# Optimization experiments

Hardware: AMD Instinct MI355X
Metric: run time of the kernel (lower is better)

Reference implementation:

```python
import jax, jax.numpy as jnp
import numpy as np

HID = 512
HEADS = 8
HD = HID // HEADS  # 64


def setup_inputs() -> dict:
    key = jax.random.key(0)
    ks = jax.random.split(key, 16)
    B, LQ, LK = 2, 384, 384
    s_in = 1.0 / np.sqrt(HID)
    s_hd = 1.0 / np.sqrt(HD)
    return {
        "query": jax.random.normal(ks[0], (B, LQ, HID), jnp.float32),
        "key":   jax.random.normal(ks[1], (B, LK, HID), jnp.float32),
        "value": jax.random.normal(ks[2], (B, LK, HID), jnp.float32),
        # linear weights stored as (in, out) so y = x @ W + b
        "Wq": jax.random.uniform(ks[3], (HID, HID), jnp.float32, -s_in, s_in),
        "bq": jnp.zeros((HID,), jnp.float32),
        "Wk": jax.random.uniform(ks[4], (HID, HID), jnp.float32, -s_in, s_in),
        "bk": jnp.zeros((HID,), jnp.float32),
        "Wv": jax.random.uniform(ks[5], (HID, HID), jnp.float32, -s_in, s_in),
        "bv": jnp.zeros((HID,), jnp.float32),
        "Ww": jax.random.uniform(ks[6], (HD, HD), jnp.float32, -s_hd, s_hd),
        "bw": jnp.zeros((HD,), jnp.float32),
        "Wu": jax.random.uniform(ks[7], (HD, HD), jnp.float32, -s_hd, s_hd),
        "bu": jnp.zeros((HD,), jnp.float32),
        "vv": jax.random.uniform(ks[8], (HD,), jnp.float32, -s_hd, s_hd),
        "Wo": jax.random.uniform(ks[9], (HID, HID), jnp.float32, -s_in, s_in),
        "bo": jnp.zeros((HID,), jnp.float32),
    }


def reference(query, key, value, Wq, bq, Wk, bk, Wv, bv, Ww, bw, Wu, bu, vv, Wo, bo):
    B, LQ, _ = query.shape
    LK = key.shape[1]
    scale = jnp.sqrt(jnp.asarray(HD, query.dtype))

    def split_heads(x, L):
        return x.reshape(B, L, HEADS, HD).transpose(0, 2, 1, 3)  # [B,H,L,hd]

    Q = split_heads(query @ Wq + bq, LQ)
    K = split_heads(key @ Wk + bk, LK)
    V = split_heads(value @ Wv + bv, LK)

    qW = Q @ Ww + bw            # [B,H,Lq,hd]
    kU = K @ Wu + bu            # [B,H,Lk,hd]
    # additive energy: tanh(W(Q)+U(K)) . vv  -> [B,H,Lq,Lk]
    e = jnp.tanh(qW[:, :, :, None, :] + kU[:, :, None, :, :])  # [B,H,Lq,Lk,hd]
    energy = jnp.einsum('bhqkd,d->bhqk', e, vv) / scale

    attention = jax.nn.softmax(energy, axis=-1)
    x = jnp.einsum('bhqk,bhkd->bhqd', attention, V)
    x = x.transpose(0, 2, 1, 3).reshape(B, LQ, HID)
    x = x @ Wo + bo
    return (x, attention)
```

## Files before the change

### kernel.cpp

```cpp
#include <hip/hip_runtime.h>

#define HID 512
#define HEADS 8
#define HD 64
#define BATCH 2
#define SEQ 384
#define MROWS (BATCH * SEQ)
#define KT_N 48
#define APACK_S8 (48 * KT_N * 64)
#define BPACK_S8 (32 * KT_N * 64)

#define C1 2.8853900817779268f
#define SSCL 0.18033688011112043f

typedef __attribute__((ext_vector_type(8))) short s8v;
typedef __attribute__((ext_vector_type(4))) float f4v;

__device__ __forceinline__ unsigned short bf16_rne(float x) {
    union { float f; unsigned u; } v; v.f = x;
    unsigned r = v.u + 0x7FFFu + ((v.u >> 16) & 1u);
    return (unsigned short)(r >> 16);
}
__device__ __forceinline__ float bf16_val(unsigned short h) {
    union { float f; unsigned u; } v; v.u = ((unsigned)h) << 16; return v.f;
}

__global__ __launch_bounds__(256) void prep_kernel(
    const float* __restrict__ Wq, const float* __restrict__ bq,
    const float* __restrict__ Wk, const float* __restrict__ bk,
    const float* __restrict__ Ww, const float* __restrict__ bw,
    const float* __restrict__ Wu, const float* __restrict__ bu,
    const float* __restrict__ vv,
    float* __restrict__ wqe, float* __restrict__ wke,
    float* __restrict__ bqe, float* __restrict__ bke,
    float* __restrict__ vv2)
{
    int tid = blockIdx.x * 256 + threadIdx.x;
    if (tid < 262144) {
        int i = tid >> 9, n = tid & 511, h = n >> 6, j = n & 63;
        const float* wrow = Wq + i * HID + h * HD;
        float s = 0.f;
        #pragma unroll 8
        for (int t = 0; t < 64; ++t) s = fmaf(wrow[t], Ww[t * 64 + j], s);
        wqe[tid] = s;
    } else if (tid < 524288) {
        int idx = tid - 262144;
        int i = idx >> 9, n = idx & 511, h = n >> 6, j = n & 63;
        const float* wrow = Wk + i * HID + h * HD;
        float s = 0.f;
        #pragma unroll 8
        for (int t = 0; t < 64; ++t) s = fmaf(wrow[t], Wu[t * 64 + j], s);
        wke[idx] = s;
    } else if (tid < 524800) {
        int n = tid - 524288, h = n >> 6, j = n & 63;
        float s = bw[j];
        for (int t = 0; t < 64; ++t) s = fmaf(bq[h * 64 + t], Ww[t * 64 + j], s);
        bqe[n] = s;
    } else if (tid < 525312) {
        int n = tid - 524800, h = n >> 6, j = n & 63;
        float s = bu[j];
        for (int t = 0; t < 64; ++t) s = fmaf(bk[h * 64 + t], Wu[t * 64 + j], s);
        bke[n] = s;
    } else if (tid < 525376) {
        int d = tid - 525312;
        vv2[d] = -2.0f * vv[d];
    }
}

__device__ __forceinline__ void pack_a_one(const float* __restrict__ src,
                                           s8v* __restrict__ dst, int rem)
{
    int g = rem & 63, m = rem >> 6;
    const float4* sp = (const float4*)(src + (size_t)m * HID + g * 8);
    float4 v0 = sp[0], v1 = sp[1];
    float vals[8] = {v0.x, v0.y, v0.z, v0.w, v1.x, v1.y, v1.z, v1.w};
    s8v hi, lo;
    #pragma unroll
    for (int j = 0; j < 8; ++j) {
        unsigned short h = bf16_rne(vals[j]);
        hi[j] = (short)h;
        lo[j] = (short)bf16_rne(vals[j] - bf16_val(h));
    }
    int mt = m >> 4, kt = g >> 2;
    int lanei = (m & 15) | ((g & 3) << 4);
    size_t base = ((size_t)mt * KT_N) * 64 + lanei;
    dst[base + (size_t)kt * 64]        = hi;
    dst[base + (size_t)(16 + kt) * 64] = hi;
    dst[base + (size_t)(32 + kt) * 64] = lo;
}

__global__ __launch_bounds__(256) void pack_a3_kernel(
    const float* __restrict__ q, const float* __restrict__ k, const float* __restrict__ v,
    s8v* __restrict__ Aq, s8v* __restrict__ Ak, s8v* __restrict__ Av)
{
    int bx = blockIdx.x;
    int p = bx / 192;
    int rem = (bx % 192) * 256 + threadIdx.x;
    const float* src = (p == 0) ? q : (p == 1) ? k : v;
    s8v* dst = (p == 0) ? Aq : (p == 1) ? Ak : Av;
    pack_a_one(src, dst, rem);
}

__global__ __launch_bounds__(256) void pack_a1_kernel(
    const float* __restrict__ x, s8v* __restrict__ Ax)
{
    pack_a_one(x, Ax, blockIdx.x * 256 + threadIdx.x);
}

__device__ __forceinline__ void pack_w_one(const float* __restrict__ W,
                                           s8v* __restrict__ dst, int rem)
{
    int kg = rem >> 9, n = rem & 511;
    s8v hi, lo;
    #pragma unroll
    for (int j = 0; j < 8; ++j) {
        float x = W[(size_t)(kg * 8 + j) * HID + n];
        unsigned short h = bf16_rne(x);
        hi[j] = (short)h;
        lo[j] = (short)bf16_rne(x - bf16_val(h));
    }
    int nt = n >> 4, kt = kg >> 2;
    int lanei = (n & 15) | ((kg & 3) << 4);
    size_t base = ((size_t)nt * KT_N) * 64 + lanei;
    dst[base + (size_t)kt * 64]        = hi;
    dst[base + (size_t)(16 + kt) * 64] = lo;
    dst[base + (size_t)(32 + kt) * 64] = hi;
}

__global__ __launch_bounds__(256) void pack_w_kernel(
    const float* __restrict__ w0, const float* __restrict__ w1,
    const float* __restrict__ w2, const float* __restrict__ w3,
    s8v* __restrict__ B0, s8v* __restrict__ B1,
    s8v* __restrict__ B2, s8v* __restrict__ B3)
{
    int bx = blockIdx.x;
    int p = bx >> 7;
    int rem = (bx & 127) * 256 + threadIdx.x;
    const float* W = (p == 0) ? w0 : (p == 1) ? w1 : (p == 2) ? w2 : w3;
    s8v* dst = (p == 0) ? B0 : (p == 1) ? B1 : (p == 2) ? B2 : B3;
    pack_w_one(W, dst, rem);
}

template <int MODE>
__device__ __forceinline__ void mfma_gemm_body(
    const s8v* __restrict__ Ap, const s8v* __restrict__ Bp,
    const float* __restrict__ bias, float* __restrict__ out,
    int bm, int bn)
{
    int tid = threadIdx.x;
    int w = __builtin_amdgcn_readfirstlane(tid >> 6);
    int lane = tid & 63;
    int mt0 = bm * 4 + (w & 1) * 2;
    int nt0 = bn * 4 + (w >> 1) * 2;

    const s8v* a0p = Ap + (size_t)(mt0 * KT_N) * 64 + lane;
    const s8v* a1p = a0p + (size_t)KT_N * 64;
    const s8v* b0p = Bp + (size_t)(nt0 * KT_N) * 64 + lane;
    const s8v* b1p = b0p + (size_t)KT_N * 64;

    f4v acc00 = {0.f, 0.f, 0.f, 0.f};
    f4v acc01 = {0.f, 0.f, 0.f, 0.f};
    f4v acc10 = {0.f, 0.f, 0.f, 0.f};
    f4v acc11 = {0.f, 0.f, 0.f, 0.f};

    s8v xa0 = a0p[0], xa1 = a1p[0], xb0 = b0p[0], xb1 = b1p[0];
    #pragma unroll 1
    for (int kt = 0; kt < KT_N; kt += 2) {
        int o1 = (kt + 1) * 64;
        s8v ya0 = a0p[o1], ya1 = a1p[o1], yb0 = b0p[o1], yb1 = b1p[o1];
        acc00 = __builtin_amdgcn_mfma_f32_16x16x32_bf16(xa0, xb0, acc00, 0, 0, 0);
        acc01 = __builtin_amdgcn_mfma_f32_16x16x32_bf16(xa0, xb1, acc01, 0, 0, 0);
        acc10 = __builtin_amdgcn_mfma_f32_16x16x32_bf16(xa1, xb0, acc10, 0, 0, 0);
        acc11 = __builtin_amdgcn_mfma_f32_16x16x32_bf16(xa1, xb1, acc11, 0, 0, 0);
        int o2 = (kt + 2 < KT_N) ? (kt + 2) * 64 : 0;
        xa0 = a0p[o2]; xa1 = a1p[o2]; xb0 = b0p[o2]; xb1 = b1p[o2];
        acc00 = __builtin_amdgcn_mfma_f32_16x16x32_bf16(ya0, yb0, acc00, 0, 0, 0);
        acc01 = __builtin_amdgcn_mfma_f32_16x16x32_bf16(ya0, yb1, acc01, 0, 0, 0);
        acc10 = __builtin_amdgcn_mfma_f32_16x16x32_bf16(ya1, yb0, acc10, 0, 0, 0);
        acc11 = __builtin_amdgcn_mfma_f32_16x16x32_bf16(ya1, yb1, acc11, 0, 0, 0);
    }

    int quad = lane >> 4, c16 = lane & 15;
    int col0 = nt0 * 16 + c16, col1 = col0 + 16;
    float bias0 = bias[col0], bias1 = bias[col1];
    int row0 = mt0 * 16 + quad * 4;
    int row1 = row0 + 16;

    #pragma unroll
    for (int r = 0; r < 4; ++r) {
        float y;
        #define WR(ROW, COL, Y)                                                     \
        {                                                                           \
            float yy = (Y);                                                         \
            if (MODE != 0) yy = __builtin_amdgcn_exp2f(C1 * yy);                    \
            if (MODE == 2) {                                                        \
                int b2 = (ROW) / SEQ, kk = (ROW) - b2 * SEQ;                        \
                int hh = (COL) >> 6, dd = (COL) & 63;                               \
                out[(((size_t)((b2 * 8 + hh) * 16 + (dd >> 2)) * SEQ + kk) << 2)    \
                    + (dd & 3)] = yy;                                               \
            } else {                                                                \
                out[(size_t)(ROW) * HID + (COL)] = yy;                              \
            }                                                                       \
        }
        y = acc00[r] + bias0; WR(row0 + r, col0, y);
        y = acc01[r] + bias1; WR(row0 + r, col1, y);
        y = acc10[r] + bias0; WR(row1 + r, col0, y);
        y = acc11[r] + bias1; WR(row1 + r, col1, y);
        #undef WR
    }
}

__global__ __launch_bounds__(256) void proj3_mfma_kernel(
    const s8v* __restrict__ Aq, const s8v* __restrict__ Ak, const s8v* __restrict__ Av,
    const s8v* __restrict__ Bq, const s8v* __restrict__ Bk, const s8v* __restrict__ Bv,
    const float* __restrict__ bqe, const float* __restrict__ bke, const float* __restrict__ bv,
    float* __restrict__ Eq, float* __restrict__ Ek4, float* __restrict__ V)
{
    int p = blockIdx.z;
    if (p == 0)      mfma_gemm_body<1>(Aq, Bq, bqe, Eq,  blockIdx.x, blockIdx.y);
    else if (p == 1) mfma_gemm_body<2>(Ak, Bk, bke, Ek4, blockIdx.x, blockIdx.y);
    else             mfma_gemm_body<0>(Av, Bv, bv,  V,   blockIdx.x, blockIdx.y);
}

__global__ __launch_bounds__(256) void out_mfma_kernel(
    const s8v* __restrict__ Ax, const s8v* __restrict__ Bo,
    const float* __restrict__ bo, float* __restrict__ out)
{
    mfma_gemm_body<0>(Ax, Bo, bo, out, blockIdx.x, blockIdx.y);
}

__global__ __launch_bounds__(256, 6) void attn_kernel(
    const float* __restrict__ Eq, const float* __restrict__ Ek4,
    const float* __restrict__ V, const float* __restrict__ vv2,
    float* __restrict__ attnOut, float* __restrict__ X)
{
    __shared__ float aP[4][SEQ];

    int bh = blockIdx.y;
    int b = bh >> 3, h = bh & 7;
    int tid = threadIdx.x;
    int wave = __builtin_amdgcn_readfirstlane(tid >> 6);
    int lane = tid & 63;
    int q = blockIdx.x * 4 + wave;

    const float* eqrow = Eq + (size_t)(b * SEQ + q) * HID + h * HD;
    const float4* ekbase = (const float4*)Ek4 + (size_t)bh * 16 * SEQ + lane;

    float e[6];
    #pragma unroll
    for (int kt = 0; kt < 6; ++kt) e[kt] = 0.f;

    #pragma unroll 1
    for (int c = 0; c < 4; ++c) {
        float g[16], w[16];
        #pragma unroll
        for (int j = 0; j < 16; ++j) {
            g[j] = eqrow[c * 16 + j];
            w[j] = vv2[c * 16 + j];
        }
        const float4* ekc = ekbase + (size_t)c * 4 * SEQ;
        #pragma unroll
        for (int kt = 0; kt < 6; ++kt) {
            const float4* ekp = ekc + kt * 64;
            float4 k0 = ekp[0 * SEQ];
            float4 k1 = ekp[1 * SEQ];
            float4 k2 = ekp[2 * SEQ];
            float4 k3 = ekp[3 * SEQ];
            float r = e[kt];
            r = fmaf(w[0],  __builtin_amdgcn_rcpf(fmaf(g[0],  k0.x, 1.f)), r);
            r = fmaf(w[1],  __builtin_amdgcn_rcpf(fmaf(g[1],  k0.y, 1.f)), r);
            r = fmaf(w[2],  __builtin_amdgcn_rcpf(fmaf(g[2],  k0.z, 1.f)), r);
            r = fmaf(w[3],  __builtin_amdgcn_rcpf(fmaf(g[3],  k0.w, 1.f)), r);
            r = fmaf(w[4],  __builtin_amdgcn_rcpf(fmaf(g[4],  k1.x, 1.f)), r);
            r = fmaf(w[5],  __builtin_amdgcn_rcpf(fmaf(g[5],  k1.y, 1.f)), r);
            r = fmaf(w[6],  __builtin_amdgcn_rcpf(fmaf(g[6],  k1.z, 1.f)), r);
            r = fmaf(w[7],  __builtin_amdgcn_rcpf(fmaf(g[7],  k1.w, 1.f)), r);
            r = fmaf(w[8],  __builtin_amdgcn_rcpf(fmaf(g[8],  k2.x, 1.f)), r);
            r = fmaf(w[9],  __builtin_amdgcn_rcpf(fmaf(g[9],  k2.y, 1.f)), r);
            r = fmaf(w[10], __builtin_amdgcn_rcpf(fmaf(g[10], k2.z, 1.f)), r);
            r = fmaf(w[11], __builtin_amdgcn_rcpf(fmaf(g[11], k2.w, 1.f)), r);
            r = fmaf(w[12], __builtin_amdgcn_rcpf(fmaf(g[12], k3.x, 1.f)), r);
            r = fmaf(w[13], __builtin_amdgcn_rcpf(fmaf(g[13], k3.y, 1.f)), r);
            r = fmaf(w[14], __builtin_amdgcn_rcpf(fmaf(g[14], k3.z, 1.f)), r);
            r = fmaf(w[15], __builtin_amdgcn_rcpf(fmaf(g[15], k3.w, 1.f)), r);
            e[kt] = r;
        }
    }

    float m = e[0];
    #pragma unroll
    for (int t = 1; t < 6; ++t) m = fmaxf(m, e[t]);
    #pragma unroll
    for (int off = 1; off < 64; off <<= 1) m = fmaxf(m, __shfl_xor(m, off));
    float a[6], s = 0.f;
    #pragma unroll
    for (int t = 0; t < 6; ++t) {
        a[t] = __builtin_amdgcn_exp2f((e[t] - m) * SSCL);
        s += a[t];
    }
    #pragma unroll
    for (int off = 1; off < 64; off <<= 1) s += __shfl_xor(s, off);
    float z = __builtin_amdgcn_rcpf(s);

    size_t abase = (size_t)bh * SEQ * SEQ + (size_t)q * SEQ;
    #pragma unroll
    for (int t = 0; t < 6; ++t) {
        float av = a[t] * z;
        attnOut[abase + t * 64 + lane] = av;
        aP[wave][t * 64 + lane] = av;
    }

    int ko = lane >> 4, d4p = lane & 15;
    const float4* vb = (const float4*)&V[(size_t)b * SEQ * HID + h * HD + d4p * 4];
    float4 x = make_float4(0.f, 0.f, 0.f, 0.f);
    #pragma unroll 8
    for (int k = ko; k < SEQ; k += 4) {
        float4 v = vb[(size_t)k * (HID / 4)];
        float av = aP[wave][k];
        x.x = fmaf(av, v.x, x.x);
        x.y = fmaf(av, v.y, x.y);
        x.z = fmaf(av, v.z, x.z);
        x.w = fmaf(av, v.w, x.w);
    }
    #pragma unroll
    for (int off = 16; off < 64; off <<= 1) {
        x.x += __shfl_xor(x.x, off);
        x.y += __shfl_xor(x.y, off);
        x.z += __shfl_xor(x.z, off);
        x.w += __shfl_xor(x.w, off);
    }
    if (ko == 0) {
        *(float4*)&X[(size_t)(b * SEQ + q) * HID + h * HD + d4p * 4] = x;
    }
}

extern "C" void kernel_launch(void* const* d_in, const int* in_sizes, int n_in,
                              void* d_out, int out_size, void* d_ws, size_t ws_size,
                              hipStream_t stream)
{
    const float* query = (const float*)d_in[0];
    const float* key   = (const float*)d_in[1];
    const float* value = (const float*)d_in[2];
    const float* Wq = (const float*)d_in[3];
    const float* bq = (const float*)d_in[4];
    const float* Wk = (const float*)d_in[5];
    const float* bk = (const float*)d_in[6];
    const float* Wv = (const float*)d_in[7];
    const float* bv = (const float*)d_in[8];
    const float* Ww = (const float*)d_in[9];
    const float* bw = (const float*)d_in[10];
    const float* Wu = (const float*)d_in[11];
    const float* bu = (const float*)d_in[12];
    const float* vv = (const float*)d_in[13];
    const float* Wo = (const float*)d_in[14];
    const float* bo = (const float*)d_in[15];

    float* out_x    = (float*)d_out;
    float* out_attn = out_x + (size_t)MROWS * HID;

    float* ws  = (float*)d_ws;
    float* wqe = ws;
    float* wke = wqe + 262144;
    float* bqe = wke + 262144;
    float* bke = bqe + 512;
    float* vv2 = bke + 512;
    float* EqB = vv2 + 64;
    float* Ek4 = EqB + 393216;
    float* Vw  = Ek4 + 393216;
    float* Xw  = Vw + 393216;

    s8v* packs = (s8v*)(Xw + 393216);
    s8v* Aq = packs;
    s8v* Ak = Aq + APACK_S8;
    s8v* Av = Ak + APACK_S8;
    s8v* Ax = Av + APACK_S8;
    s8v* Bq = Ax + APACK_S8;
    s8v* Bk = Bq + BPACK_S8;
    s8v* Bv = Bk + BPACK_S8;
    s8v* Bo = Bv + BPACK_S8;

    prep_kernel<<<dim3(2053), 256, 0, stream>>>(Wq, bq, Wk, bk, Ww, bw, Wu, bu, vv,
                                                wqe, wke, bqe, bke, vv2);
    pack_w_kernel<<<dim3(512), 256, 0, stream>>>(wqe, wke, Wv, Wo, Bq, Bk, Bv, Bo);
    pack_a3_kernel<<<dim3(576), 256, 0, stream>>>(query, key, value, Aq, Ak, Av);
    proj3_mfma_kernel<<<dim3(12, 8, 3), 256, 0, stream>>>(Aq, Ak, Av, Bq, Bk, Bv,
                                                          bqe, bke, bv,
                                                          EqB, Ek4, Vw);
    attn_kernel<<<dim3(96, 16), 256, 0, stream>>>(EqB, Ek4, Vw, vv2, out_attn, Xw);
    pack_a1_kernel<<<dim3(192), 256, 0, stream>>>(Xw, Ax);
    out_mfma_kernel<<<dim3(12, 8), 256, 0, stream>>>(Ax, Bo, bo, out_x);
}
```

Baseline: 171.4 us.

## Fuse prep with input packing, shrink GEMM blocks, process two queries per wave

The input packing launch is merged into the weight-prep kernel, which removes one kernel launch. The MFMA GEMMs now run one wave per block on a finer grid, giving more blocks to spread across CUs. In the attention kernel each wave handles two query rows, so every Ek4 tile load and V load is reused twice, and the next Ek tile is prefetched. Each thread now holds more registers, so the occupancy hint drops from 6 to 4.

After: 154.2 us. -10.1%, faster.

```diff
diff --git a/kernel.cpp b/kernel.cpp
--- a/kernel.cpp
+++ b/kernel.cpp
@@ -25,7 +25,29 @@
     union { float f; unsigned u; } v; v.u = ((unsigned)h) << 16; return v.f;
 }
 
-__global__ __launch_bounds__(256) void prep_kernel(
+__device__ __forceinline__ void pack_a_one(const float* __restrict__ src,
+                                           s8v* __restrict__ dst, int rem)
+{
+    int g = rem & 63, m = rem >> 6;
+    const float4* sp = (const float4*)(src + (size_t)m * HID + g * 8);
+    float4 v0 = sp[0], v1 = sp[1];
+    float vals[8] = {v0.x, v0.y, v0.z, v0.w, v1.x, v1.y, v1.z, v1.w};
+    s8v hi, lo;
+    #pragma unroll
+    for (int j = 0; j < 8; ++j) {
+        unsigned short h = bf16_rne(vals[j]);
+        hi[j] = (short)h;
+        lo[j] = (short)bf16_rne(vals[j] - bf16_val(h));
+    }
+    int mt = m >> 4, kt = g >> 2;
+    int lanei = (m & 15) | ((g & 3) << 4);
+    size_t base = ((size_t)mt * KT_N) * 64 + lanei;
+    dst[base + (size_t)kt * 64]        = hi;
+    dst[base + (size_t)(16 + kt) * 64] = hi;
+    dst[base + (size_t)(32 + kt) * 64] = lo;
+}
+
+__global__ __launch_bounds__(256) void prep_pack_kernel(
     const float* __restrict__ Wq, const float* __restrict__ bq,
     const float* __restrict__ Wk, const float* __restrict__ bk,
     const float* __restrict__ Ww, const float* __restrict__ bw,
@@ -33,8 +55,19 @@
     const float* __restrict__ vv,
     float* __restrict__ wqe, float* __restrict__ wke,
     float* __restrict__ bqe, float* __restrict__ bke,
-    float* __restrict__ vv2)
-{
+    float* __restrict__ vv2,
+    const float* __restrict__ q, const float* __restrict__ k, const float* __restrict__ v,
+    s8v* __restrict__ Aq, s8v* __restrict__ Ak, s8v* __restrict__ Av)
+{
+    if (blockIdx.x >= 2053) {
+        int bx = blockIdx.x - 2053;
+        int p = bx / 192;
+        int rem = (bx % 192) * 256 + threadIdx.x;
+        const float* src = (p == 0) ? q : (p == 1) ? k : v;
+        s8v* dst = (p == 0) ? Aq : (p == 1) ? Ak : Av;
+        pack_a_one(src, dst, rem);
+        return;
+    }
     int tid = blockIdx.x * 256 + threadIdx.x;
     if (tid < 262144) {
         int i = tid >> 9, n = tid & 511, h = n >> 6, j = n & 63;
@@ -67,40 +100,6 @@
     }
 }
 
-__device__ __forceinline__ void pack_a_one(const float* __restrict__ src,
-                                           s8v* __restrict__ dst, int rem)
-{
-    int g = rem & 63, m = rem >> 6;
-    const float4* sp = (const float4*)(src + (size_t)m * HID + g * 8);
-    float4 v0 = sp[0], v1 = sp[1];
-    float vals[8] = {v0.x, v0.y, v0.z, v0.w, v1.x, v1.y, v1.z, v1.w};
-    s8v hi, lo;
-    #pragma unroll
-    for (int j = 0; j < 8; ++j) {
-        unsigned short h = bf16_rne(vals[j]);
-        hi[j] = (short)h;
-        lo[j] = (short)bf16_rne(vals[j] - bf16_val(h));
-    }
-    int mt = m >> 4, kt = g >> 2;
-    int lanei = (m & 15) | ((g & 3) << 4);
-    size_t base = ((size_t)mt * KT_N) * 64 + lanei;
-    dst[base + (size_t)kt * 64]        = hi;
-    dst[base + (size_t)(16 + kt) * 64] = hi;
-    dst[base + (size_t)(32 + kt) * 64] = lo;
-}
-
-__global__ __launch_bounds__(256) void pack_a3_kernel(
-    const float* __restrict__ q, const float* __restrict__ k, const float* __restrict__ v,
-    s8v* __restrict__ Aq, s8v* __restrict__ Ak, s8v* __restrict__ Av)
-{
-    int bx = blockIdx.x;
-    int p = bx / 192;
-    int rem = (bx % 192) * 256 + threadIdx.x;
-    const float* src = (p == 0) ? q : (p == 1) ? k : v;
-    s8v* dst = (p == 0) ? Aq : (p == 1) ? Ak : Av;
-    pack_a_one(src, dst, rem);
-}
-
 __global__ __launch_bounds__(256) void pack_a1_kernel(
     const float* __restrict__ x, s8v* __restrict__ Ax)
 {
@@ -145,13 +144,9 @@
 __device__ __forceinline__ void mfma_gemm_body(
     const s8v* __restrict__ Ap, const s8v* __restrict__ Bp,
     const float* __restrict__ bias, float* __restrict__ out,
-    int bm, int bn)
-{
-    int tid = threadIdx.x;
-    int w = __builtin_amdgcn_readfirstlane(tid >> 6);
-    int lane = tid & 63;
-    int mt0 = bm * 4 + (w & 1) * 2;
-    int nt0 = bn * 4 + (w >> 1) * 2;
+    int mt0, int nt0)
+{
+    int lane = threadIdx.x & 63;
 
     const s8v* a0p = Ap + (size_t)(mt0 * KT_N) * 64 + lane;
     const s8v* a1p = a0p + (size_t)KT_N * 64;
@@ -210,127 +205,139 @@
     }
 }
 
-__global__ __launch_bounds__(256) void proj3_mfma_kernel(
+__global__ __launch_bounds__(64) void proj3_mfma_kernel(
     const s8v* __restrict__ Aq, const s8v* __restrict__ Ak, const s8v* __restrict__ Av,
     const s8v* __restrict__ Bq, const s8v* __restrict__ Bk, const s8v* __restrict__ Bv,
     const float* __restrict__ bqe, const float* __restrict__ bke, const float* __restrict__ bv,
     float* __restrict__ Eq, float* __restrict__ Ek4, float* __restrict__ V)
 {
     int p = blockIdx.z;
-    if (p == 0)      mfma_gemm_body<1>(Aq, Bq, bqe, Eq,  blockIdx.x, blockIdx.y);
-    else if (p == 1) mfma_gemm_body<2>(Ak, Bk, bke, Ek4, blockIdx.x, blockIdx.y);
-    else             mfma_gemm_body<0>(Av, Bv, bv,  V,   blockIdx.x, blockIdx.y);
-}
-
-__global__ __launch_bounds__(256) void out_mfma_kernel(
+    int mt0 = blockIdx.x * 2, nt0 = blockIdx.y * 2;
+    if (p == 0)      mfma_gemm_body<1>(Aq, Bq, bqe, Eq,  mt0, nt0);
+    else if (p == 1) mfma_gemm_body<2>(Ak, Bk, bke, Ek4, mt0, nt0);
+    else             mfma_gemm_body<0>(Av, Bv, bv,  V,   mt0, nt0);
+}
+
+__global__ __launch_bounds__(64) void out_mfma_kernel(
     const s8v* __restrict__ Ax, const s8v* __restrict__ Bo,
     const float* __restrict__ bo, float* __restrict__ out)
 {
-    mfma_gemm_body<0>(Ax, Bo, bo, out, blockIdx.x, blockIdx.y);
-}
-
-__global__ __launch_bounds__(256, 6) void attn_kernel(
+    mfma_gemm_body<0>(Ax, Bo, bo, out, blockIdx.x * 2, blockIdx.y * 2);
+}
+
+__global__ __launch_bounds__(256, 4) void attn_kernel(
     const float* __restrict__ Eq, const float* __restrict__ Ek4,
     const float* __restrict__ V, const float* __restrict__ vv2,
     float* __restrict__ attnOut, float* __restrict__ X)
 {
-    __shared__ float aP[4][SEQ];
+    __shared__ float2 aP[4][SEQ];
 
     int bh = blockIdx.y;
     int b = bh >> 3, h = bh & 7;
     int tid = threadIdx.x;
     int wave = __builtin_amdgcn_readfirstlane(tid >> 6);
     int lane = tid & 63;
-    int q = blockIdx.x * 4 + wave;
-
-    const float* eqrow = Eq + (size_t)(b * SEQ + q) * HID + h * HD;
+    int q0 = blockIdx.x * 8 + wave * 2, q1 = q0 + 1;
+
+    const float* eq0 = Eq + (size_t)(b * SEQ + q0) * HID + h * HD;
+    const float* eq1 = eq0 + HID;
     const float4* ekbase = (const float4*)Ek4 + (size_t)bh * 16 * SEQ + lane;
 
-    float e[6];
-    #pragma unroll
-    for (int kt = 0; kt < 6; ++kt) e[kt] = 0.f;
+    float e0[6], e1[6];
+    #pragma unroll
+    for (int t = 0; t < 6; ++t) { e0[t] = 0.f; e1[t] = 0.f; }
 
     #pragma unroll 1
     for (int c = 0; c < 4; ++c) {
-        float g[16], w[16];
+        float g0[16], g1[16], w[16];
         #pragma unroll
         for (int j = 0; j < 16; ++j) {
-            g[j] = eqrow[c * 16 + j];
-            w[j] = vv2[c * 16 + j];
+            g0[j] = eq0[c * 16 + j];
+            g1[j] = eq1[c * 16 + j];
+            w[j]  = vv2[c * 16 + j];
         }
         const float4* ekc = ekbase + (size_t)c * 4 * SEQ;
+        float4 k0 = ekc[0 * SEQ], k1 = ekc[1 * SEQ];
+        float4 k2 = ekc[2 * SEQ], k3 = ekc[3 * SEQ];
         #pragma unroll
         for (int kt = 0; kt < 6; ++kt) {
-            const float4* ekp = ekc + kt * 64;
-            float4 k0 = ekp[0 * SEQ];
-            float4 k1 = ekp[1 * SEQ];
-            float4 k2 = ekp[2 * SEQ];
-            float4 k3 = ekp[3 * SEQ];
-            float r = e[kt];
-            r = fmaf(w[0],  __builtin_amdgcn_rcpf(fmaf(g[0],  k0.x, 1.f)), r);
-            r = fmaf(w[1],  __builtin_amdgcn_rcpf(fmaf(g[1],  k0.y, 1.f)), r);
-            r = fmaf(w[2],  __builtin_amdgcn_rcpf(fmaf(g[2],  k0.z, 1.f)), r);
-            r = fmaf(w[3],  __builtin_amdgcn_rcpf(fmaf(g[3],  k0.w, 1.f)), r);
-            r = fmaf(w[4],  __builtin_amdgcn_rcpf(fmaf(g[4],  k1.x, 1.f)), r);
-            r = fmaf(w[5],  __builtin_amdgcn_rcpf(fmaf(g[5],  k1.y, 1.f)), r);
-            r = fmaf(w[6],  __builtin_amdgcn_rcpf(fmaf(g[6],  k1.z, 1.f)), r);
-            r = fmaf(w[7],  __builtin_amdgcn_rcpf(fmaf(g[7],  k1.w, 1.f)), r);
-            r = fmaf(w[8],  __builtin_amdgcn_rcpf(fmaf(g[8],  k2.x, 1.f)), r);
-            r = fmaf(w[9],  __builtin_amdgcn_rcpf(fmaf(g[9],  k2.y, 1.f)), r);
-            r = fmaf(w[10], __builtin_amdgcn_rcpf(fmaf(g[10], k2.z, 1.f)), r);
-            r = fmaf(w[11], __builtin_amdgcn_rcpf(fmaf(g[11], k2.w, 1.f)), r);
-            r = fmaf(w[12], __builtin_amdgcn_rcpf(fmaf(g[12], k3.x, 1.f)), r);
-            r = fmaf(w[13], __builtin_amdgcn_rcpf(fmaf(g[13], k3.y, 1.f)), r);
-            r = fmaf(w[14], __builtin_amdgcn_rcpf(fmaf(g[14], k3.z, 1.f)), r);
-            r = fmaf(w[15], __builtin_amdgcn_rcpf(fmaf(g[15], k3.w, 1.f)), r);
-            e[kt] = r;
+            float4 n0, n1, n2, n3;
+            if (kt < 5) {
+                const float4* np = ekc + (kt + 1) * 64;
+                n0 = np[0 * SEQ]; n1 = np[1 * SEQ];
+                n2 = np[2 * SEQ]; n3 = np[3 * SEQ];
+            }
+            float r0 = e0[kt], r1 = e1[kt];
+            #define EN(J, KV)                                                      \
+            {                                                                      \
+                float t0 = __builtin_amdgcn_rcpf(fmaf(g0[J], (KV), 1.f));          \
+                float t1 = __builtin_amdgcn_rcpf(fmaf(g1[J], (KV), 1.f));          \
+                r0 = fmaf(w[J], t0, r0);                                           \
+                r1 = fmaf(w[J], t1, r1);                                           \
+            }
+            EN(0,  k0.x) EN(1,  k0.y) EN(2,  k0.z) EN(3,  k0.w)
+            EN(4,  k1.x) EN(5,  k1.y) EN(6,  k1.z) EN(7,  k1.w)
+            EN(8,  k2.x) EN(9,  k2.y) EN(10, k2.z) EN(11, k2.w)
+            EN(12, k3.x) EN(13, k3.y) EN(14, k3.z) EN(15, k3.w)
+            #undef EN
+            e0[kt] = r0; e1[kt] = r1;
+            k0 = n0; k1 = n1; k2 = n2; k3 = n3;
         }
     }
 
-    float m = e[0];
-    #pragma unroll
-    for (int t = 1; t < 6; ++t) m = fmaxf(m, e[t]);
-    #pragma unroll
-    for (int off = 1; off < 64; off <<= 1) m = fmaxf(m, __shfl_xor(m, off));
-    float a[6], s = 0.f;
+    float m0 = e0[0], m1 = e1[0];
+    #pragma unroll
+    for (int t = 1; t < 6; ++t) { m0 = fmaxf(m0, e0[t]); m1 = fmaxf(m1, e1[t]); }
+    #pragma unroll
+    for (int off = 1; off < 64; off <<= 1) {
+        m0 = fmaxf(m0, __shfl_xor(m0, off));
+        m1 = fmaxf(m1, __shfl_xor(m1, off));
+    }
+    float a0[6], a1[6], s0 = 0.f, s1 = 0.f;
     #pragma unroll
     for (int t = 0; t < 6; ++t) {
-        a[t] = __builtin_amdgcn_exp2f((e[t] - m) * SSCL);
-        s += a[t];
-    }
-    #pragma unroll
-    for (int off = 1; off < 64; off <<= 1) s += __shfl_xor(s, off);
-    float z = __builtin_amdgcn_rcpf(s);
-
-    size_t abase = (size_t)bh * SEQ * SEQ + (size_t)q * SEQ;
+        a0[t] = __builtin_amdgcn_exp2f((e0[t] - m0) * SSCL); s0 += a0[t];
+        a1[t] = __builtin_amdgcn_exp2f((e1[t] - m1) * SSCL); s1 += a1[t];
+    }
+    #pragma unroll
+    for (int off = 1; off < 64; off <<= 1) {
+        s0 += __shfl_xor(s0, off);
+        s1 += __shfl_xor(s1, off);
+    }
+    float z0 = __builtin_amdgcn_rcpf(s0), z1 = __builtin_amdgcn_rcpf(s1);
+
+    size_t abase = (size_t)bh * SEQ * SEQ + (size_t)q0 * SEQ;
     #pragma unroll
     for (int t = 0; t < 6; ++t) {
-        float av = a[t] * z;
-        attnOut[abase + t * 64 + lane] = av;
-        aP[wave][t * 64 + lane] = av;
+        float v0 = a0[t] * z0, v1 = a1[t] * z1;
+        attnOut[abase + t * 64 + lane] = v0;
+        attnOut[abase + SEQ + t * 64 + lane] = v1;
+        aP[wave][t * 64 + lane] = make_float2(v0, v1);
     }
 
     int ko = lane >> 4, d4p = lane & 15;
     const float4* vb = (const float4*)&V[(size_t)b * SEQ * HID + h * HD + d4p * 4];
-    float4 x = make_float4(0.f, 0.f, 0.f, 0.f);
+    float4 x0 = make_float4(0.f, 0.f, 0.f, 0.f);
+    float4 x1 = make_float4(0.f, 0.f, 0.f, 0.f);
     #pragma unroll 8
     for (int k = ko; k < SEQ; k += 4) {
         float4 v = vb[(size_t)k * (HID / 4)];
-        float av = aP[wave][k];
-        x.x = fmaf(av, v.x, x.x);
-        x.y = fmaf(av, v.y, x.y);
-        x.z = fmaf(av, v.z, x.z);
-        x.w = fmaf(av, v.w, x.w);
+        float2 a = aP[wave][k];
+        x0.x = fmaf(a.x, v.x, x0.x); x0.y = fmaf(a.x, v.y, x0.y);
+        x0.z = fmaf(a.x, v.z, x0.z); x0.w = fmaf(a.x, v.w, x0.w);
+        x1.x = fmaf(a.y, v.x, x1.x); x1.y = fmaf(a.y, v.y, x1.y);
+        x1.z = fmaf(a.y, v.z, x1.z); x1.w = fmaf(a.y, v.w, x1.w);
     }
     #pragma unroll
     for (int off = 16; off < 64; off <<= 1) {
-        x.x += __shfl_xor(x.x, off);
-        x.y += __shfl_xor(x.y, off);
-        x.z += __shfl_xor(x.z, off);
-        x.w += __shfl_xor(x.w, off);
+        x0.x += __shfl_xor(x0.x, off); x0.y += __shfl_xor(x0.y, off);
+        x0.z += __shfl_xor(x0.z, off); x0.w += __shfl_xor(x0.w, off);
+        x1.x += __shfl_xor(x1.x, off); x1.y += __shfl_xor(x1.y, off);
+        x1.z += __shfl_xor(x1.z, off); x1.w += __shfl_xor(x1.w, off);
     }
     if (ko == 0) {
-        *(float4*)&X[(size_t)(b * SEQ + q) * HID + h * HD + d4p * 4] = x;
+        *(float4*)&X[(size_t)(b * SEQ + q0) * HID + h * HD + d4p * 4] = x0;
+        *(float4*)&X[(size_t)(b * SEQ + q1) * HID + h * HD + d4p * 4] = x1;
     }
 }
 
@@ -379,14 +386,15 @@
     s8v* Bv = Bk + BPACK_S8;
     s8v* Bo = Bv + BPACK_S8;
 
-    prep_kernel<<<dim3(2053), 256, 0, stream>>>(Wq, bq, Wk, bk, Ww, bw, Wu, bu, vv,
-                                                wqe, wke, bqe, bke, vv2);
+    prep_pack_kernel<<<dim3(2629), 256, 0, stream>>>(
+        Wq, bq, Wk, bk, Ww, bw, Wu, bu, vv,
+        wqe, wke, bqe, bke, vv2,
+        query, key, value, Aq, Ak, Av);
     pack_w_kernel<<<dim3(512), 256, 0, stream>>>(wqe, wke, Wv, Wo, Bq, Bk, Bv, Bo);
-    pack_a3_kernel<<<dim3(576), 256, 0, stream>>>(query, key, value, Aq, Ak, Av);
-    proj3_mfma_kernel<<<dim3(12, 8, 3), 256, 0, stream>>>(Aq, Ak, Av, Bq, Bk, Bv,
+    proj3_mfma_kernel<<<dim3(24, 16, 3), 64, 0, stream>>>(Aq, Ak, Av, Bq, Bk, Bv,
                                                           bqe, bke, bv,
                                                           EqB, Ek4, Vw);
-    attn_kernel<<<dim3(96, 16), 256, 0, stream>>>(EqB, Ek4, Vw, vv2, out_attn, Xw);
+    attn_kernel<<<dim3(48, 16), 256, 0, stream>>>(EqB, Ek4, Vw, vv2, out_attn, Xw);
     pack_a1_kernel<<<dim3(192), 256, 0, stream>>>(Xw, Ax);
-    out_mfma_kernel<<<dim3(12, 8), 256, 0, stream>>>(Ax, Bo, bo, out_x);
-}
+    out_mfma_kernel<<<dim3(24, 16), 64, 0, stream>>>(Ax, Bo, bo, out_x);
+}
```
